# Performance work log

Hardware: AMD Instinct MI355X
Metric: run time of the kernel (lower is better)

## Reference

```python
import jax, jax.numpy as jnp
import numpy as np

# Static module configuration (matches init_kwargs)
B, CIN, COUT, K, H, W = 4, 32, 32, 3, 128, 128
UM = 2                      # um_dim: 2D vector fields
NW = ((K - 1) // 2) * 4     # num_weights = radius*4 = 4


def setup_inputs() -> dict:
    key = jax.random.key(0)
    k1, k2, k3 = jax.random.split(key, 3)
    params = jax.random.normal(k1, (COUT, CIN, NW, 4), jnp.float32)
    basis = jax.random.normal(k2, (NW, 4, K, K, UM, UM), jnp.float32)
    # Replicate the init-time scaling of the torch module:
    # std over the (non-zero) outer-product kernel, then scale params and basis.
    init_kernel = jnp.einsum('abcd,cdefgh->abcdefgh', params, basis)
    stds = jnp.std(init_kernel)  # random basis -> all entries nonzero
    scaler = jnp.sqrt(0.6 / (np.sqrt(CIN) * (K ** 2) * stds))
    params = params * scaler
    basis = basis * scaler
    bias_term = jnp.ones((1, COUT, 2, 1, 1), jnp.float32) / 100.0
    b = jnp.float32(0.01)
    xx = jax.random.normal(k3, (B, CIN * UM, H, W), jnp.float32)
    return {'xx': xx, 'params': params, 'basis': basis,
            'bias_term': bias_term, 'b': b}


def _forward(xx, params, basis, bias_term, b):
    Bn, C, Hh, Ww = xx.shape
    I, O = CIN, COUT
    # --- get_kernel: einsum + transposes -> conv weight (O*2, I*2, K, K) ---
    Kr = jnp.einsum('abcd,cdefgh->abefgh', params, basis)      # (O,I,K,K,2,2)
    kernel = jnp.transpose(Kr, (0, 4, 1, 5, 2, 3)).reshape(O * 2, I * 2, K, K)
    # --- unfold with replicate padding: P[b,c,kh,kw,h,w] ---
    xp = jnp.pad(xx, ((0, 0), (0, 0), (1, 1), (1, 1)), mode='edge')
    P = jnp.stack([xp[:, :, i:i + Hh, j:j + Ww]
                   for i in range(K) for j in range(K)], axis=2)
    P = P.reshape(Bn, C, K, K, Hh, Ww)
    # --- per-window mean subtraction over (input_channels, kh, kw) ---
    P5 = P.reshape(Bn, I, UM, K, K, Hh, Ww)
    avgs = P5.mean(axis=(1, 3, 4), keepdims=True)              # (B,1,2,1,1,H,W)
    P = (P5 - avgs).reshape(Bn, C, K, K, Hh, Ww)
    avgs = avgs[:, :, :, 0, 0]                                 # (B,1,2,H,W)
    # --- strided conv2d on the blown-up grid == this einsum:
    # big[b,c,3h+di,3w+dj] = P[b,c,kh=dj,kw=di,h,w], so kernel (di,dj)=(p,q)
    # pairs with patch (kh=q, kw=p).
    out = jnp.einsum('bcqphw,ocpq->bohw', P, kernel)           # (B,O*2,H,W)
    out = out.reshape(Bn, O, 2, Hh, Ww) + bias_term
    # --- 'relu' vector activation: normalize, zero where norm <= b ---
    norm = jnp.sqrt(out[:, :, 0] ** 2 + out[:, :, 1] ** 2)[:, :, None]
    out = jnp.where(norm - b <= 0.0, 0.0, out / norm)
    # --- add_mean ---
    out = out + avgs
    return out.reshape(Bn, O * 2, Hh, Ww)


def reference(xx, params, basis, bias_term, b):
    return _forward(xx, params, basis, bias_term, b)
```

## Files before the change

### kernel.cpp

```cpp
#include <hip/hip_runtime.h>

#define BN 4
#define CH 64
#define HH 128
#define WW 128
#define PIX (HH*WW)

#define OFF_WL  0
#define OFF_S   36864
#define OFF_CS  36992

__device__ __forceinline__ int iclamp(int v, int lo, int hi) {
    return v < lo ? lo : (v > hi ? hi : v);
}

__global__ __launch_bounds__(256) void k_prep(const float* __restrict__ params,
                                              const float* __restrict__ basis,
                                              const float* __restrict__ x,
                                              float* __restrict__ Wl,
                                              float* __restrict__ S,
                                              float* __restrict__ cs) {
    int bx = blockIdx.x;
    if (bx < 144) {
        int idx = bx * 256 + threadIdx.x;
        int oc  = idx & 63;
        int tap = (idx >> 6) % 9;
        int c   = idx / 576;
        int q = tap / 3, p = tap % 3;
        int o = oc >> 1, g = oc & 1;
        int i = c >> 1, u = c & 1;
        float s = 0.f;
        #pragma unroll
        for (int n = 0; n < 4; ++n)
            #pragma unroll
            for (int d = 0; d < 4; ++d)
                s = fmaf(params[((o * 32 + i) * 4 + n) * 4 + d],
                         basis[((((n * 4 + d) * 3 + p) * 3 + q) * 2 + g) * 2 + u], s);
        Wl[(((oc >> 4) * 64 + c) * 9 + tap) * 16 + (oc & 15)] = s;
    } else if (bx == 144) {
        int t = threadIdx.x;
        if (t < 128) {
            int u = t >> 6, oc = t & 63;
            int o = oc >> 1, g = oc & 1;
            float s = 0.f;
            #pragma unroll
            for (int nd = 0; nd < 16; ++nd) {
                int n = nd >> 2, d = nd & 3;
                float pa = 0.f;
                for (int i = 0; i < 32; ++i)
                    pa += params[((o * 32 + i) * 4 + n) * 4 + d];
                float sb = 0.f;
                #pragma unroll
                for (int e = 0; e < 3; ++e)
                    #pragma unroll
                    for (int f = 0; f < 3; ++f)
                        sb += basis[((((n * 4 + d) * 3 + e) * 3 + f) * 2 + g) * 2 + u];
                s = fmaf(pa, sb, s);
            }
            S[t] = s;
        }
    } else {
        int idx = (bx - 145) * 256 + threadIdx.x;
        int pq  = idx & (PIX / 4 - 1);
        int u   = (idx >> 12) & 1;
        int b   = idx >> 13;
        const float4* xb = (const float4*)x;
        float4 s = make_float4(0.f, 0.f, 0.f, 0.f);
        #pragma unroll
        for (int i = 0; i < 32; ++i) {
            float4 v = xb[(size_t)(b * CH + 2 * i + u) * (PIX / 4) + pq];
            s.x += v.x; s.y += v.y; s.z += v.z; s.w += v.w;
        }
        ((float4*)cs)[(b * 2 + u) * (PIX / 4) + pq] = s;
    }
}

__global__ __launch_bounds__(256, 4) void k_main(
    const float* __restrict__ x,
    const float* __restrict__ Wl,
    const float* __restrict__ S,
    const float* __restrict__ bias,
    const float* __restrict__ cs,
    const float* __restrict__ bptr,
    float* __restrict__ out)
{
    int tile = blockIdx.x;
    int ocg  = blockIdx.y;
    int b    = blockIdx.z;
    int ty = threadIdx.x >> 4, tx = threadIdx.x & 15;
    int h = (tile >> 3) * 16 + ty;
    int w = (tile & 7) * 16 + tx;

    int hm = h > 0 ? h - 1 : 0, hp = h < HH - 1 ? h + 1 : HH - 1;
    int wm = w > 0 ? w - 1 : 0, wp = w < WW - 1 ? w + 1 : WW - 1;
    int rowoff[3] = { hm * WW, h * WW, hp * WW };
    int coloff[3] = { wm, w, wp };
    int off[9];
    #pragma unroll
    for (int r = 0; r < 3; ++r)
        #pragma unroll
        for (int p = 0; p < 3; ++p)
            off[r * 3 + p] = rowoff[r] + coloff[p];

    float acc[16];
    #pragma unroll
    for (int j = 0; j < 16; ++j) acc[j] = 0.f;

    const float* xb = x + (size_t)b * CH * PIX;
    const float* wc = Wl + (size_t)ocg * 64 * 144;

    float xA[9], xB[9];
    #pragma unroll
    for (int k = 0; k < 9; ++k) xA[k] = xb[off[k]];
    #pragma unroll
    for (int k = 0; k < 9; ++k) xB[k] = xb[PIX + off[k]];

    for (int c = 0; c < CH; c += 2) {
        int c2 = c + 2 < CH ? c + 2 : CH - 1;
        int c3 = c + 3 < CH ? c + 3 : CH - 1;
        const float* p2 = xb + (size_t)c2 * PIX;
        const float* p3 = xb + (size_t)c3 * PIX;
        float xN0[9], xN1[9];
        #pragma unroll
        for (int k = 0; k < 9; ++k) xN0[k] = p2[off[k]];
        #pragma unroll
        for (int k = 0; k < 9; ++k) xN1[k] = p3[off[k]];

        #pragma unroll
        for (int t = 0; t < 9; ++t) {
            float xt = xA[t];
            #pragma unroll
            for (int j = 0; j < 16; ++j)
                acc[j] = fmaf(xt, wc[t * 16 + j], acc[j]);
        }
        #pragma unroll
        for (int t = 0; t < 9; ++t) {
            float xt = xB[t];
            #pragma unroll
            for (int j = 0; j < 16; ++j)
                acc[j] = fmaf(xt, wc[144 + t * 16 + j], acc[j]);
        }

        #pragma unroll
        for (int k = 0; k < 9; ++k) { xA[k] = xN0[k]; xB[k] = xN1[k]; }
        wc += 288;
    }

    int pix = h * WW + w;
    const float* c0p = cs + (size_t)(b * 2 + 0) * PIX;
    const float* c1p = cs + (size_t)(b * 2 + 1) * PIX;
    int r0 = rowoff[0], r1 = rowoff[1], r2 = rowoff[2];
    float a0 = (c0p[r0 + wm] + c0p[r0 + w] + c0p[r0 + wp]
              + c0p[r1 + wm] + c0p[r1 + w] + c0p[r1 + wp]
              + c0p[r2 + wm] + c0p[r2 + w] + c0p[r2 + wp]) * (1.0f / 288.0f);
    float a1 = (c1p[r0 + wm] + c1p[r0 + w] + c1p[r0 + wp]
              + c1p[r1 + wm] + c1p[r1 + w] + c1p[r1 + wp]
              + c1p[r2 + wm] + c1p[r2 + w] + c1p[r2 + wp]) * (1.0f / 288.0f);
    float bthr = bptr[0];

    float* ob = out + (size_t)b * CH * PIX + pix;
    #pragma unroll
    for (int j = 0; j < 16; j += 2) {
        int oc = ocg * 16 + j;
        float t0 = acc[j]     - a0 * S[oc]     - a1 * S[64 + oc]     + bias[oc];
        float t1 = acc[j + 1] - a0 * S[oc + 1] - a1 * S[64 + oc + 1] + bias[oc + 1];
        float n = sqrtf(t0 * t0 + t1 * t1);
        float r0v, r1v;
        if (n - bthr <= 0.f) { r0v = 0.f; r1v = 0.f; }
        else { r0v = t0 / n; r1v = t1 / n; }
        ob[(size_t)oc * PIX]       = r0v + a0;
        ob[(size_t)(oc + 1) * PIX] = r1v + a1;
    }
}

extern "C" void kernel_launch(void* const* d_in, const int* in_sizes, int n_in,
                              void* d_out, int out_size, void* d_ws, size_t ws_size,
                              hipStream_t stream) {
    const float* xx     = (const float*)d_in[0];
    const float* params = (const float*)d_in[1];
    const float* basis  = (const float*)d_in[2];
    const float* bias   = (const float*)d_in[3];
    const float* bptr   = (const float*)d_in[4];
    float* out = (float*)d_out;
    float* ws  = (float*)d_ws;

    float* Wl  = ws + OFF_WL;
    float* S   = ws + OFF_S;
    float* cs  = ws + OFF_CS;

    k_prep<<<273, 256, 0, stream>>>(params, basis, xx, Wl, S, cs);

    dim3 grid(64, 4, BN);
    k_main<<<grid, 256, 0, stream>>>(xx, Wl, S, bias, cs, bptr, out);
}
```

Before: 144.7 us.

## Split input channels across two thread halves with shared-memory reduction

```diff
diff --git a/kernel.cpp b/kernel.cpp
--- a/kernel.cpp
+++ b/kernel.cpp
@@ -75,7 +75,7 @@
     }
 }
 
-__global__ __launch_bounds__(256, 4) void k_main(
+__global__ __launch_bounds__(256, 8) void k_main(
     const float* __restrict__ x,
     const float* __restrict__ Wl,
     const float* __restrict__ S,
@@ -84,11 +84,16 @@
     const float* __restrict__ bptr,
     float* __restrict__ out)
 {
+    __shared__ float red[16 * 128];
+
     int tile = blockIdx.x;
     int ocg  = blockIdx.y;
     int b    = blockIdx.z;
-    int ty = threadIdx.x >> 4, tx = threadIdx.x & 15;
-    int h = (tile >> 3) * 16 + ty;
+    int t    = threadIdx.x;
+    int px   = t & 127;
+    int half = t >> 7;
+    int ty = px >> 4, tx = px & 15;
+    int h = (tile >> 3) * 8 + ty;
     int w = (tile & 7) * 16 + tx;
 
     int hm = h > 0 ? h - 1 : 0, hp = h < HH - 1 ? h + 1 : HH - 1;
@@ -106,70 +111,65 @@
     #pragma unroll
     for (int j = 0; j < 16; ++j) acc[j] = 0.f;
 
-    const float* xb = x + (size_t)b * CH * PIX;
-    const float* wc = Wl + (size_t)ocg * 64 * 144;
+    const float* xb = x + (size_t)b * CH * PIX + (size_t)(half * 32) * PIX;
+    const float* wc = Wl + (size_t)ocg * 64 * 144 + (size_t)(half * 32) * 144;
 
-    float xA[9], xB[9];
+    float xA[9];
     #pragma unroll
     for (int k = 0; k < 9; ++k) xA[k] = xb[off[k]];
-    #pragma unroll
-    for (int k = 0; k < 9; ++k) xB[k] = xb[PIX + off[k]];
 
-    for (int c = 0; c < CH; c += 2) {
-        int c2 = c + 2 < CH ? c + 2 : CH - 1;
-        int c3 = c + 3 < CH ? c + 3 : CH - 1;
-        const float* p2 = xb + (size_t)c2 * PIX;
-        const float* p3 = xb + (size_t)c3 * PIX;
-        float xN0[9], xN1[9];
+    for (int c = 0; c < 32; ++c) {
+        const float* xn = xb + (size_t)(c + 1 < 32 ? c + 1 : c) * PIX;
+        float xN[9];
         #pragma unroll
-        for (int k = 0; k < 9; ++k) xN0[k] = p2[off[k]];
+        for (int k = 0; k < 9; ++k) xN[k] = xn[off[k]];
+
+        const float* wt = wc + c * 144;
         #pragma unroll
-        for (int k = 0; k < 9; ++k) xN1[k] = p3[off[k]];
-
-        #pragma unroll
-        for (int t = 0; t < 9; ++t) {
-            float xt = xA[t];
+        for (int tap = 0; tap < 9; ++tap) {
+            float xt = xA[tap];
             #pragma unroll
             for (int j = 0; j < 16; ++j)
-                acc[j] = fmaf(xt, wc[t * 16 + j], acc[j]);
+                acc[j] = fmaf(xt, wt[tap * 16 + j], acc[j]);
         }
         #pragma unroll
-        for (int t = 0; t < 9; ++t) {
-            float xt = xB[t];
-            #pragma unroll
-            for (int j = 0; j < 16; ++j)
-                acc[j] = fmaf(xt, wc[144 + t * 16 + j], acc[j]);
-        }
-
-        #pragma unroll
-        for (int k = 0; k < 9; ++k) { xA[k] = xN0[k]; xB[k] = xN1[k]; }
-        wc += 288;
+        for (int k = 0; k < 9; ++k) xA[k] = xN[k];
     }
 
-    int pix = h * WW + w;
-    const float* c0p = cs + (size_t)(b * 2 + 0) * PIX;
-    const float* c1p = cs + (size_t)(b * 2 + 1) * PIX;
-    int r0 = rowoff[0], r1 = rowoff[1], r2 = rowoff[2];
-    float a0 = (c0p[r0 + wm] + c0p[r0 + w] + c0p[r0 + wp]
-              + c0p[r1 + wm] + c0p[r1 + w] + c0p[r1 + wp]
-              + c0p[r2 + wm] + c0p[r2 + w] + c0p[r2 + wp]) * (1.0f / 288.0f);
-    float a1 = (c1p[r0 + wm] + c1p[r0 + w] + c1p[r0 + wp]
-              + c1p[r1 + wm] + c1p[r1 + w] + c1p[r1 + wp]
-              + c1p[r2 + wm] + c1p[r2 + w] + c1p[r2 + wp]) * (1.0f / 288.0f);
-    float bthr = bptr[0];
+    if (half) {
+        #pragma unroll
+        for (int j = 0; j < 16; ++j) red[j * 128 + px] = acc[j];
+    }
+    __syncthreads();
+    if (!half) {
+        #pragma unroll
+        for (int j = 0; j < 16; ++j) acc[j] += red[j * 128 + px];
 
-    float* ob = out + (size_t)b * CH * PIX + pix;
-    #pragma unroll
-    for (int j = 0; j < 16; j += 2) {
-        int oc = ocg * 16 + j;
-        float t0 = acc[j]     - a0 * S[oc]     - a1 * S[64 + oc]     + bias[oc];
-        float t1 = acc[j + 1] - a0 * S[oc + 1] - a1 * S[64 + oc + 1] + bias[oc + 1];
-        float n = sqrtf(t0 * t0 + t1 * t1);
-        float r0v, r1v;
-        if (n - bthr <= 0.f) { r0v = 0.f; r1v = 0.f; }
-        else { r0v = t0 / n; r1v = t1 / n; }
-        ob[(size_t)oc * PIX]       = r0v + a0;
-        ob[(size_t)(oc + 1) * PIX] = r1v + a1;
+        int pix = h * WW + w;
+        const float* c0p = cs + (size_t)(b * 2 + 0) * PIX;
+        const float* c1p = cs + (size_t)(b * 2 + 1) * PIX;
+        int r0 = rowoff[0], r1 = rowoff[1], r2 = rowoff[2];
+        float a0 = (c0p[r0 + wm] + c0p[r0 + w] + c0p[r0 + wp]
+                  + c0p[r1 + wm] + c0p[r1 + w] + c0p[r1 + wp]
+                  + c0p[r2 + wm] + c0p[r2 + w] + c0p[r2 + wp]) * (1.0f / 288.0f);
+        float a1 = (c1p[r0 + wm] + c1p[r0 + w] + c1p[r0 + wp]
+                  + c1p[r1 + wm] + c1p[r1 + w] + c1p[r1 + wp]
+                  + c1p[r2 + wm] + c1p[r2 + w] + c1p[r2 + wp]) * (1.0f / 288.0f);
+        float bthr = bptr[0];
+
+        float* ob = out + (size_t)b * CH * PIX + pix;
+        #pragma unroll
+        for (int j = 0; j < 16; j += 2) {
+            int oc = ocg * 16 + j;
+            float t0 = acc[j]     - a0 * S[oc]     - a1 * S[64 + oc]     + bias[oc];
+            float t1 = acc[j + 1] - a0 * S[oc + 1] - a1 * S[64 + oc + 1] + bias[oc + 1];
+            float n = sqrtf(t0 * t0 + t1 * t1);
+            float r0v, r1v;
+            if (n - bthr <= 0.f) { r0v = 0.f; r1v = 0.f; }
+            else { r0v = t0 / n; r1v = t1 / n; }
+            ob[(size_t)oc * PIX]       = r0v + a0;
+            ob[(size_t)(oc + 1) * PIX] = r1v + a1;
+        }
     }
 }
 
@@ -190,6 +190,6 @@
 
     k_prep<<<273, 256, 0, stream>>>(params, basis, xx, Wl, S, cs);
 
-    dim3 grid(64, 4, BN);
+    dim3 grid(128, 4, BN);
     k_main<<<grid, 256, 0, stream>>>(xx, Wl, S, bias, cs, bptr, out);
 }
```

Measured after the change: 388.7 us. 169% more time.
